# Kernel optimization log

Hardware: AMD Instinct MI355X
Metric: run time of the kernel (lower is better)

The kernel has to match this reference:

```python
import jax, jax.numpy as jnp
import numpy as np


def _grid_sample_bilinear(plane, xy):
    """torch grid_sample, mode=bilinear, padding_mode=zeros, align_corners=True.
    plane: (C, H, W); xy: (N, 2) with xy[:,0]->W axis, xy[:,1]->H axis, in [-1,1].
    Returns (N, C)."""
    C, H, W = plane.shape
    x = (xy[:, 0] + 1.0) * 0.5 * (W - 1)  # pixel coords, align_corners=True
    y = (xy[:, 1] + 1.0) * 0.5 * (H - 1)
    x0 = jnp.floor(x)
    y0 = jnp.floor(y)
    wx = x - x0
    wy = y - y0
    x0i = x0.astype(jnp.int32)
    y0i = y0.astype(jnp.int32)

    def gather(yi, xi):
        valid = ((yi >= 0) & (yi < H) & (xi >= 0) & (xi < W)).astype(plane.dtype)
        v = plane[:, jnp.clip(yi, 0, H - 1), jnp.clip(xi, 0, W - 1)]  # (C, N)
        return v * valid  # zeros padding

    out = (gather(y0i, x0i) * ((1 - wx) * (1 - wy))
           + gather(y0i, x0i + 1) * (wx * (1 - wy))
           + gather(y0i + 1, x0i) * ((1 - wx) * wy)
           + gather(y0i + 1, x0i + 1) * (wx * wy))  # (C, N)
    return out.T  # (N, C)


def _sample_plane_xtytxy(coords3d, plane_xtyt, plane_xy):
    # coords3d: (N, 3) = (x, y, t)
    xy = coords3d[:, 0:2]
    yt = coords3d[:, 1:3]
    xt = coords3d[:, jnp.array([0, 2])]
    f_xt = _grid_sample_bilinear(plane_xtyt[0], xt)
    f_yt = _grid_sample_bilinear(plane_xtyt[1], yt)
    f_xy = _grid_sample_bilinear(plane_xy[0], xy)
    return f_xt + f_yt + f_xy  # (N, feat_dim)  [sum over the 3 planes]


def setup_inputs() -> dict:
    key = jax.random.key(0)
    ks = jax.random.split(key, 10)
    N, FD = 2_000_000, 16
    x_res = [128, 256, 512]
    t_res = [16, 32, 64]
    inp = {
        "coords": jax.random.uniform(ks[0], (N, 3), jnp.float32, minval=-1.0, maxval=1.0),
    }
    for i, (rx, rt) in enumerate(zip(x_res, t_res)):
        inp[f"xtyt_{i}"] = jax.random.normal(ks[1 + 2 * i], (2, FD, rt, rx), jnp.float32) * 0.001
        inp[f"xy_{i}"] = jax.random.normal(ks[2 + 2 * i], (1, FD, rx, rx), jnp.float32) * 0.001
    width, out_dim = 32, 2
    inp["w1"] = jax.random.normal(ks[7], (FD * 3, width), jnp.float32) * (1.0 / np.sqrt(FD * 3))
    inp["b1"] = jnp.zeros((width,), jnp.float32)
    inp["w2"] = jax.random.normal(ks[8], (width, out_dim), jnp.float32) * (1.0 / np.sqrt(width))
    inp["b2"] = jnp.zeros((out_dim,), jnp.float32)
    return inp


def reference(coords, xtyt_0, xy_0, xtyt_1, xy_1, xtyt_2, xy_2, w1, b1, w2, b2):
    feats = jnp.concatenate([
        _sample_plane_xtytxy(coords, xtyt_0, xy_0),
        _sample_plane_xtytxy(coords, xtyt_1, xy_1),
        _sample_plane_xtytxy(coords, xtyt_2, xy_2),
    ], axis=-1)  # (N, 48)
    h = jax.nn.leaky_relu(feats @ w1 + b1, negative_slope=0.01)
    return jax.nn.sigmoid(h @ w2 + b2)  # (N, 2) in [0, 1]
```

## Files before the change

### kernel.cpp

```cpp
#include <hip/hip_runtime.h>
#include <hip/hip_bf16.h>

#define FD 16

typedef unsigned int uint32_t_;
typedef __attribute__((ext_vector_type(4))) unsigned int u32x4;

__device__ __forceinline__ unsigned char enc_e4m3(float v) {
  float sv = v * 32768.0f;
  unsigned int bits = __float_as_uint(sv);
  unsigned int s = (bits >> 24) & 0x80u;
  float a = fabsf(sv);
  if (a >= 448.0f) return (unsigned char)(s | 0x7Eu);
  unsigned int tb = __float_as_uint(a * 0x1p-120f);
  unsigned int lsb = (tb >> 20) & 1u;
  tb += 0x7FFFFu + lsb;
  unsigned int em = (tb >> 20) & 0x7Fu;
  if (em > 0x7Eu) em = 0x7Eu;
  return (unsigned char)(s | em);
}

__device__ __forceinline__ float dec_e4m3_raw(unsigned int b) {
  unsigned int u = ((b & 0x80u) << 24) | ((b & 0x7Fu) << 20);
  return __uint_as_float(u);
}

__global__ __launch_bounds__(256) void pack_kernel(
    const float* __restrict__ in, unsigned char* __restrict__ out,
    int P, int H, int W)
{
  int idx = blockIdx.x * blockDim.x + threadIdx.x;
  int total = P * H * W;
  if (idx >= total) return;
  int w  = idx % W;
  int ph = idx / W;
  int h  = ph % H;
  int p  = ph / H;
  int hw = H * W;
  const float* src = in + ((size_t)(p * FD) * H + h) * (size_t)W + w;
  unsigned int words[4];
#pragma unroll
  for (int g = 0; g < 4; ++g) {
    unsigned int acc = 0;
#pragma unroll
    for (int c = 0; c < 4; ++c) {
      unsigned int b = enc_e4m3(src[(size_t)(4 * g + c) * hw]);
      acc |= b << (8 * c);
    }
    words[g] = acc;
  }
  u32x4* dst = (u32x4*)(out + (size_t)idx * FD);
  u32x4 v; v.x = words[0]; v.y = words[1]; v.z = words[2]; v.w = words[3];
  *dst = v;
}

template<int H, int W>
__device__ __forceinline__ void sample_add(
    const unsigned char* __restrict__ base, float u, float v, float* __restrict__ f)
{
  float gx = ((u + 1.0f) * 0.5f) * (float)(W - 1);
  float gy = ((v + 1.0f) * 0.5f) * (float)(H - 1);
  float fx0 = floorf(gx), fy0 = floorf(gy);
  float wx = gx - fx0, wy = gy - fy0;
  int x0 = (int)fx0, y0 = (int)fy0;
  int x0c = min(max(x0, 0), W - 1);
  int x1c = min(max(x0 + 1, 0), W - 1);
  int y0c = min(max(y0, 0), H - 1);
  int y1c = min(max(y0 + 1, 0), H - 1);
  float w00 = (1.0f - wx) * (1.0f - wy);
  float w01 = wx * (1.0f - wy);
  float w10 = (1.0f - wx) * wy;
  float w11 = wx * wy;
  const u32x4* p00 = (const u32x4*)(base + ((y0c * W + x0c) << 4));
  const u32x4* p01 = (const u32x4*)(base + ((y0c * W + x1c) << 4));
  const u32x4* p10 = (const u32x4*)(base + ((y1c * W + x0c) << 4));
  const u32x4* p11 = (const u32x4*)(base + ((y1c * W + x1c) << 4));
  u32x4 A = *p00, B = *p01, C = *p10, D = *p11;
#pragma unroll
  for (int g = 0; g < 4; ++g) {
    unsigned int wa = A[g], wb = B[g], wc = C[g], wd = D[g];
#pragma unroll
    for (int c = 0; c < 4; ++c) {
      int sh = 8 * c;
      float va = dec_e4m3_raw((wa >> sh) & 0xFFu);
      float vb = dec_e4m3_raw((wb >> sh) & 0xFFu);
      float vc = dec_e4m3_raw((wc >> sh) & 0xFFu);
      float vd = dec_e4m3_raw((wd >> sh) & 0xFFu);
      f[4 * g + c] += w00 * va + w01 * vb + w10 * vc + w11 * vd;
    }
  }
}

constexpr int SZ0_XT = 2 * 16 * 128 * FD;
constexpr int SZ0_XY = 128 * 128 * FD;
constexpr int SZ1_XT = 2 * 32 * 256 * FD;
constexpr int SZ1_XY = 256 * 256 * FD;
constexpr int SZ2_XT = 2 * 64 * 512 * FD;
constexpr int SZ2_XY = 512 * 512 * FD;
constexpr int OFF0_XT = 0;
constexpr int OFF0_XY = OFF0_XT + SZ0_XT;
constexpr int OFF1_XT = OFF0_XY + SZ0_XY;
constexpr int OFF1_XY = OFF1_XT + SZ1_XT;
constexpr int OFF2_XT = OFF1_XY + SZ1_XY;
constexpr int OFF2_XY = OFF2_XT + SZ2_XT;

__global__ __launch_bounds__(256) void triplane_kernel(
    const float* __restrict__ coords,
    const unsigned char* __restrict__ planes,
    const float* __restrict__ w1, const float* __restrict__ b1,
    const float* __restrict__ w2, const float* __restrict__ b2,
    float* __restrict__ out, int N)
{
  __shared__ float s_w1[48 * 32];
  __shared__ float s_b1[32];
  __shared__ float s_w2[32 * 2];
  __shared__ float s_b2[2];
  for (int i = threadIdx.x; i < 48 * 32; i += 256) s_w1[i] = w1[i] * 0x1p105f;
  if (threadIdx.x < 32) s_b1[threadIdx.x] = b1[threadIdx.x];
  if (threadIdx.x < 64) s_w2[threadIdx.x] = w2[threadIdx.x];
  if (threadIdx.x < 2)  s_b2[threadIdx.x] = b2[threadIdx.x];
  __syncthreads();

  int n = blockIdx.x * blockDim.x + threadIdx.x;
  if (n >= N) return;

  float x = coords[3 * (size_t)n + 0];
  float y = coords[3 * (size_t)n + 1];
  float t = coords[3 * (size_t)n + 2];

  float f[48];
#pragma unroll
  for (int i = 0; i < 48; ++i) f[i] = 0.0f;

  sample_add<16, 128>(planes + OFF0_XT,                 x, t, f + 0);
  sample_add<16, 128>(planes + OFF0_XT + 16 * 128 * FD, y, t, f + 0);
  sample_add<128, 128>(planes + OFF0_XY,                x, y, f + 0);
  sample_add<32, 256>(planes + OFF1_XT,                 x, t, f + 16);
  sample_add<32, 256>(planes + OFF1_XT + 32 * 256 * FD, y, t, f + 16);
  sample_add<256, 256>(planes + OFF1_XY,                x, y, f + 16);
  sample_add<64, 512>(planes + OFF2_XT,                 x, t, f + 32);
  sample_add<64, 512>(planes + OFF2_XT + 64 * 512 * FD, y, t, f + 32);
  sample_add<512, 512>(planes + OFF2_XY,                x, y, f + 32);

  float h[32];
#pragma unroll
  for (int j = 0; j < 32; ++j) h[j] = s_b1[j];
#pragma unroll
  for (int k = 0; k < 48; ++k) {
    float fk = f[k];
#pragma unroll
    for (int j = 0; j < 32; ++j) h[j] = fmaf(fk, s_w1[k * 32 + j], h[j]);
  }
  float o0 = s_b2[0], o1 = s_b2[1];
#pragma unroll
  for (int j = 0; j < 32; ++j) {
    float hj = h[j];
    hj = hj > 0.0f ? hj : 0.01f * hj;
    o0 = fmaf(hj, s_w2[j * 2 + 0], o0);
    o1 = fmaf(hj, s_w2[j * 2 + 1], o1);
  }
  out[2 * (size_t)n + 0] = 1.0f / (1.0f + __expf(-o0));
  out[2 * (size_t)n + 1] = 1.0f / (1.0f + __expf(-o1));
}

extern "C" void kernel_launch(void* const* d_in, const int* in_sizes, int n_in,
                              void* d_out, int out_size, void* d_ws, size_t ws_size,
                              hipStream_t stream) {
  const float* coords = (const float*)d_in[0];
  const float* xtyt0  = (const float*)d_in[1];
  const float* xy0    = (const float*)d_in[2];
  const float* xtyt1  = (const float*)d_in[3];
  const float* xy1    = (const float*)d_in[4];
  const float* xtyt2  = (const float*)d_in[5];
  const float* xy2    = (const float*)d_in[6];
  const float* w1     = (const float*)d_in[7];
  const float* b1     = (const float*)d_in[8];
  const float* w2     = (const float*)d_in[9];
  const float* b2     = (const float*)d_in[10];

  unsigned char* planes = (unsigned char*)d_ws;
  const int N = in_sizes[0] / 3;

  auto launch_pk = [&](const float* src, int off, int P, int H, int W) {
    int total = P * H * W;
    int blocks = (total + 255) / 256;
    hipLaunchKernelGGL(pack_kernel, dim3(blocks), dim3(256), 0, stream,
                       src, planes + off, P, H, W);
  };
  launch_pk(xtyt0, OFF0_XT, 2, 16, 128);
  launch_pk(xy0,   OFF0_XY, 1, 128, 128);
  launch_pk(xtyt1, OFF1_XT, 2, 32, 256);
  launch_pk(xy1,   OFF1_XY, 1, 256, 256);
  launch_pk(xtyt2, OFF2_XT, 2, 64, 512);
  launch_pk(xy2,   OFF2_XY, 1, 512, 512);

  int blocks = (N + 255) / 256;
  hipLaunchKernelGGL(triplane_kernel, dim3(blocks), dim3(256), 0, stream,
                     coords, planes, w1, b1, w2, b2, (float*)d_out, N);
}
```

Before: 418.8 us.

## Use hardware fp8 packed conversion and packed-FMA math for sampling and MLP

Replaces the manual bit-manipulation fp8 decode with the hardware cvt_pk_f32_fp8 instruction. Sampling accumulation and the first MLP layer now use two-wide packed FMAs. The MLP is interleaved per resolution level so that only 16 features are live at a time, which cuts register pressure. The w1 scale changes from 2^105 to 2^-15 because the hardware decode yields real e4m3 values. This relies on the packed encoding matching the hardware's e4m3 format, including saturation and NaN behaviour.

```diff
diff --git a/kernel.cpp b/kernel.cpp
--- a/kernel.cpp
+++ b/kernel.cpp
@@ -3,7 +3,8 @@
 
 #define FD 16
 
-typedef unsigned int uint32_t_;
+typedef __attribute__((ext_vector_type(2))) float f32x2;
+typedef __attribute__((ext_vector_type(4))) float f32x4;
 typedef __attribute__((ext_vector_type(4))) unsigned int u32x4;
 
 __device__ __forceinline__ unsigned char enc_e4m3(float v) {
@@ -20,11 +21,6 @@
   return (unsigned char)(s | em);
 }
 
-__device__ __forceinline__ float dec_e4m3_raw(unsigned int b) {
-  unsigned int u = ((b & 0x80u) << 24) | ((b & 0x7Fu) << 20);
-  return __uint_as_float(u);
-}
-
 __global__ __launch_bounds__(256) void pack_kernel(
     const float* __restrict__ in, unsigned char* __restrict__ out,
     int P, int H, int W)
@@ -49,14 +45,13 @@
     }
     words[g] = acc;
   }
-  u32x4* dst = (u32x4*)(out + (size_t)idx * FD);
   u32x4 v; v.x = words[0]; v.y = words[1]; v.z = words[2]; v.w = words[3];
-  *dst = v;
+  *(u32x4*)(out + (size_t)idx * FD) = v;
 }
 
 template<int H, int W>
 __device__ __forceinline__ void sample_add(
-    const unsigned char* __restrict__ base, float u, float v, float* __restrict__ f)
+    const unsigned char* __restrict__ base, float u, float v, f32x2* __restrict__ f)
 {
   float gx = ((u + 1.0f) * 0.5f) * (float)(W - 1);
   float gy = ((v + 1.0f) * 0.5f) * (float)(H - 1);
@@ -71,22 +66,44 @@
   float w01 = wx * (1.0f - wy);
   float w10 = (1.0f - wx) * wy;
   float w11 = wx * wy;
-  const u32x4* p00 = (const u32x4*)(base + ((y0c * W + x0c) << 4));
-  const u32x4* p01 = (const u32x4*)(base + ((y0c * W + x1c) << 4));
-  const u32x4* p10 = (const u32x4*)(base + ((y1c * W + x0c) << 4));
-  const u32x4* p11 = (const u32x4*)(base + ((y1c * W + x1c) << 4));
-  u32x4 A = *p00, B = *p01, C = *p10, D = *p11;
+  u32x4 A = *(const u32x4*)(base + ((y0c * W + x0c) << 4));
+  u32x4 B = *(const u32x4*)(base + ((y0c * W + x1c) << 4));
+  u32x4 C = *(const u32x4*)(base + ((y1c * W + x0c) << 4));
+  u32x4 D = *(const u32x4*)(base + ((y1c * W + x1c) << 4));
+  f32x2 vw00 = {w00, w00}, vw01 = {w01, w01}, vw10 = {w10, w10}, vw11 = {w11, w11};
 #pragma unroll
   for (int g = 0; g < 4; ++g) {
-    unsigned int wa = A[g], wb = B[g], wc = C[g], wd = D[g];
-#pragma unroll
-    for (int c = 0; c < 4; ++c) {
-      int sh = 8 * c;
-      float va = dec_e4m3_raw((wa >> sh) & 0xFFu);
-      float vb = dec_e4m3_raw((wb >> sh) & 0xFFu);
-      float vc = dec_e4m3_raw((wc >> sh) & 0xFFu);
-      float vd = dec_e4m3_raw((wd >> sh) & 0xFFu);
-      f[4 * g + c] += w00 * va + w01 * vb + w10 * vc + w11 * vd;
+    f32x2 acc0 = f[2 * g + 0];
+    f32x2 acc1 = f[2 * g + 1];
+    acc0 = __builtin_elementwise_fma(vw00, __builtin_amdgcn_cvt_pk_f32_fp8(A[g], false), acc0);
+    acc1 = __builtin_elementwise_fma(vw00, __builtin_amdgcn_cvt_pk_f32_fp8(A[g], true ), acc1);
+    acc0 = __builtin_elementwise_fma(vw01, __builtin_amdgcn_cvt_pk_f32_fp8(B[g], false), acc0);
+    acc1 = __builtin_elementwise_fma(vw01, __builtin_amdgcn_cvt_pk_f32_fp8(B[g], true ), acc1);
+    acc0 = __builtin_elementwise_fma(vw10, __builtin_amdgcn_cvt_pk_f32_fp8(C[g], false), acc0);
+    acc1 = __builtin_elementwise_fma(vw10, __builtin_amdgcn_cvt_pk_f32_fp8(C[g], true ), acc1);
+    acc0 = __builtin_elementwise_fma(vw11, __builtin_amdgcn_cvt_pk_f32_fp8(D[g], false), acc0);
+    acc1 = __builtin_elementwise_fma(vw11, __builtin_amdgcn_cvt_pk_f32_fp8(D[g], true ), acc1);
+    f[2 * g + 0] = acc0;
+    f[2 * g + 1] = acc1;
+  }
+}
+
+__device__ __forceinline__ void mlp_chunk(
+    const f32x2* __restrict__ fr, const float* __restrict__ s_w1, int row0,
+    f32x2* __restrict__ h2)
+{
+#pragma unroll
+  for (int k = 0; k < 16; ++k) {
+    float fk = fr[k >> 1][k & 1];
+    f32x2 fk2 = {fk, fk};
+    const f32x4* wrow = (const f32x4*)(s_w1 + (row0 + k) * 32);
+#pragma unroll
+    for (int q = 0; q < 8; ++q) {
+      f32x4 w4 = wrow[q];
+      f32x2 wlo = {w4.x, w4.y};
+      f32x2 whi = {w4.z, w4.w};
+      h2[2 * q + 0] = __builtin_elementwise_fma(fk2, wlo, h2[2 * q + 0]);
+      h2[2 * q + 1] = __builtin_elementwise_fma(fk2, whi, h2[2 * q + 1]);
     }
   }
 }
@@ -111,13 +128,16 @@
     const float* __restrict__ w2, const float* __restrict__ b2,
     float* __restrict__ out, int N)
 {
-  __shared__ float s_w1[48 * 32];
+  __shared__ __align__(16) float s_w1[48 * 32];
   __shared__ float s_b1[32];
-  __shared__ float s_w2[32 * 2];
+  __shared__ float s_w2t[2 * 32];
   __shared__ float s_b2[2];
-  for (int i = threadIdx.x; i < 48 * 32; i += 256) s_w1[i] = w1[i] * 0x1p105f;
+  for (int i = threadIdx.x; i < 48 * 32; i += 256) s_w1[i] = w1[i] * 0x1p-15f;
   if (threadIdx.x < 32) s_b1[threadIdx.x] = b1[threadIdx.x];
-  if (threadIdx.x < 64) s_w2[threadIdx.x] = w2[threadIdx.x];
+  if (threadIdx.x < 64) {
+    int j = threadIdx.x >> 1, c = threadIdx.x & 1;
+    s_w2t[c * 32 + j] = w2[j * 2 + c];
+  }
   if (threadIdx.x < 2)  s_b2[threadIdx.x] = b2[threadIdx.x];
   __syncthreads();
 
@@ -128,39 +148,62 @@
   float y = coords[3 * (size_t)n + 1];
   float t = coords[3 * (size_t)n + 2];
 
-  float f[48];
-#pragma unroll
-  for (int i = 0; i < 48; ++i) f[i] = 0.0f;
-
-  sample_add<16, 128>(planes + OFF0_XT,                 x, t, f + 0);
-  sample_add<16, 128>(planes + OFF0_XT + 16 * 128 * FD, y, t, f + 0);
-  sample_add<128, 128>(planes + OFF0_XY,                x, y, f + 0);
-  sample_add<32, 256>(planes + OFF1_XT,                 x, t, f + 16);
-  sample_add<32, 256>(planes + OFF1_XT + 32 * 256 * FD, y, t, f + 16);
-  sample_add<256, 256>(planes + OFF1_XY,                x, y, f + 16);
-  sample_add<64, 512>(planes + OFF2_XT,                 x, t, f + 32);
-  sample_add<64, 512>(planes + OFF2_XT + 64 * 512 * FD, y, t, f + 32);
-  sample_add<512, 512>(planes + OFF2_XY,                x, y, f + 32);
-
-  float h[32];
-#pragma unroll
-  for (int j = 0; j < 32; ++j) h[j] = s_b1[j];
-#pragma unroll
-  for (int k = 0; k < 48; ++k) {
-    float fk = f[k];
-#pragma unroll
-    for (int j = 0; j < 32; ++j) h[j] = fmaf(fk, s_w1[k * 32 + j], h[j]);
-  }
-  float o0 = s_b2[0], o1 = s_b2[1];
-#pragma unroll
-  for (int j = 0; j < 32; ++j) {
-    float hj = h[j];
-    hj = hj > 0.0f ? hj : 0.01f * hj;
-    o0 = fmaf(hj, s_w2[j * 2 + 0], o0);
-    o1 = fmaf(hj, s_w2[j * 2 + 1], o1);
-  }
-  out[2 * (size_t)n + 0] = 1.0f / (1.0f + __expf(-o0));
-  out[2 * (size_t)n + 1] = 1.0f / (1.0f + __expf(-o1));
+  f32x2 h2[16];
+#pragma unroll
+  for (int j = 0; j < 16; ++j) { h2[j][0] = s_b1[2 * j]; h2[j][1] = s_b1[2 * j + 1]; }
+
+  {
+    f32x2 fr[8];
+#pragma unroll
+    for (int i = 0; i < 8; ++i) { fr[i][0] = 0.0f; fr[i][1] = 0.0f; }
+    sample_add<16, 128>(planes + OFF0_XT,                 x, t, fr);
+    sample_add<16, 128>(planes + OFF0_XT + 16 * 128 * FD, y, t, fr);
+    sample_add<128, 128>(planes + OFF0_XY,                x, y, fr);
+    mlp_chunk(fr, s_w1, 0, h2);
+  }
+  {
+    f32x2 fr[8];
+#pragma unroll
+    for (int i = 0; i < 8; ++i) { fr[i][0] = 0.0f; fr[i][1] = 0.0f; }
+    sample_add<32, 256>(planes + OFF1_XT,                 x, t, fr);
+    sample_add<32, 256>(planes + OFF1_XT + 32 * 256 * FD, y, t, fr);
+    sample_add<256, 256>(planes + OFF1_XY,                x, y, fr);
+    mlp_chunk(fr, s_w1, 16, h2);
+  }
+  {
+    f32x2 fr[8];
+#pragma unroll
+    for (int i = 0; i < 8; ++i) { fr[i][0] = 0.0f; fr[i][1] = 0.0f; }
+    sample_add<64, 512>(planes + OFF2_XT,                 x, t, fr);
+    sample_add<64, 512>(planes + OFF2_XT + 64 * 512 * FD, y, t, fr);
+    sample_add<512, 512>(planes + OFF2_XY,                x, y, fr);
+    mlp_chunk(fr, s_w1, 32, h2);
+  }
+
+  f32x2 zero = {0.0f, 0.0f};
+  f32x2 c01 = {0.01f, 0.01f};
+#pragma unroll
+  for (int j = 0; j < 16; ++j) {
+    f32x2 hp = __builtin_elementwise_max(h2[j], zero);
+    f32x2 hn = __builtin_elementwise_min(h2[j], zero);
+    h2[j] = __builtin_elementwise_fma(c01, hn, hp);
+  }
+
+  f32x2 oa = zero, ob = zero;
+#pragma unroll
+  for (int j = 0; j < 16; ++j) {
+    f32x2 w2a = *(const f32x2*)(s_w2t + 2 * j);
+    f32x2 w2b = *(const f32x2*)(s_w2t + 32 + 2 * j);
+    oa = __builtin_elementwise_fma(h2[j], w2a, oa);
+    ob = __builtin_elementwise_fma(h2[j], w2b, ob);
+  }
+  float o0 = s_b2[0] + oa[0] + oa[1];
+  float o1 = s_b2[1] + ob[0] + ob[1];
+
+  f32x2 r;
+  r[0] = 1.0f / (1.0f + __expf(-o0));
+  r[1] = 1.0f / (1.0f + __expf(-o1));
+  *(f32x2*)(out + 2 * (size_t)n) = r;
 }
 
 extern "C" void kernel_launch(void* const* d_in, const int* in_sizes, int n_in,
```

New measurement: 353.4 us. 15.6% less time.
